# Kernel tuning notes

Hardware: AMD Instinct MI355X
Metric: run time of the kernel (lower is better)

## Reference

```python
import jax, jax.numpy as jnp
import numpy as np

EMB = 768
HEADS = 8
B, N = 8, 1024

def _ln(x, g, b, eps=1e-5):
    mu = jnp.mean(x, axis=-1, keepdims=True)
    var = jnp.mean(jnp.square(x - mu), axis=-1, keepdims=True)
    return (x - mu) * jax.lax.rsqrt(var + eps) * g + b

def setup_inputs() -> dict:
    key = jax.random.key(0)
    ks = jax.random.split(key, 8)
    s_in = 0.02
    return {
        "x": jax.random.normal(ks[0], (B, N, EMB), jnp.float32),
        "w_qkvr": jax.random.normal(ks[1], (EMB, 4 * EMB), jnp.float32) * s_in,
        "b_qkvr": jnp.zeros((4 * EMB,), jnp.float32),
        "w_proj": jax.random.normal(ks[2], (EMB, EMB), jnp.float32) * s_in,
        "b_proj": jnp.zeros((EMB,), jnp.float32),
        "ln1_g": jnp.ones((EMB,), jnp.float32),
        "ln1_b": jnp.zeros((EMB,), jnp.float32),
        "w_ff1": jax.random.normal(ks[3], (EMB, 4 * EMB), jnp.float32) * s_in,
        "b_ff1": jnp.zeros((4 * EMB,), jnp.float32),
        "w_ff2": jax.random.normal(ks[4], (4 * EMB, EMB), jnp.float32) * s_in,
        "b_ff2": jnp.zeros((EMB,), jnp.float32),
        "ln2_g": jnp.ones((EMB,), jnp.float32),
        "ln2_b": jnp.zeros((EMB,), jnp.float32),
    }

def reference(x, w_qkvr, b_qkvr, w_proj, b_proj, ln1_g, ln1_b,
              w_ff1, b_ff1, w_ff2, b_ff2, ln2_g, ln2_b):
    b, n, e = x.shape
    h = HEADS
    d = e // h
    # fused QKV+R projection; einops '(h d qkvr)' => qkvr is the INNERMOST factor
    qkvr = (x @ w_qkvr + b_qkvr).reshape(b, n, h, d, 4)
    qkvr = jnp.transpose(qkvr, (4, 0, 2, 1, 3))  # [4, b, h, n, d]
    q, k, v, r = qkvr[0], qkvr[1], qkvr[2], qkvr[3]
    energy = jnp.einsum('bhqd,bhkd->bhqk', q, k)
    # quirk: softmax of UNSCALED logits, then divide by sqrt(emb_size) AFTER
    att = jax.nn.softmax(energy, axis=-1) / jnp.sqrt(jnp.float32(e))
    out = jnp.einsum('bhqk,bhkd->bhqd', att, v)
    out = out * r  # elementwise r-gate
    out = jnp.transpose(out, (0, 2, 1, 3)).reshape(b, n, e)
    out = out @ w_proj + b_proj
    x1 = _ln(out + x, ln1_g, ln1_b)  # residual then post-LayerNorm
    ff = jax.nn.gelu(x1 @ w_ff1 + b_ff1, approximate=False) @ w_ff2 + b_ff2
    return _ln(ff + x1, ln2_g, ln2_b)
```

## Files before the change

### kernel.cpp

```cpp
#include <hip/hip_runtime.h>
#include <math.h>


typedef __bf16 bf16_t;
typedef __bf16 bf16x4 __attribute__((ext_vector_type(4)));
typedef __bf16 bf16x8 __attribute__((ext_vector_type(8)));
typedef float f32x4 __attribute__((ext_vector_type(4)));

#define EMB   768
#define HEADS 8
#define DHEAD 96
#define BATCH 8
#define SEQ   1024
#define ROWS  (BATCH * SEQ)

__device__ __forceinline__ void load16_lds(const bf16_t* g, bf16_t* l) {
    __builtin_amdgcn_global_load_lds(
        (__attribute__((address_space(1))) unsigned int*)g,
        (__attribute__((address_space(3))) unsigned int*)l,
        16, 0, 0);
}


__global__ void cvt_bf16_kernel(const float* __restrict__ in, bf16_t* __restrict__ out, int n) {
    int stride = gridDim.x * blockDim.x;
    for (int i = blockIdx.x * blockDim.x + threadIdx.x; i < n; i += stride)
        out[i] = (bf16_t)in[i];
}

__global__ void transpose_cvt_kernel(const float* __restrict__ in, bf16_t* __restrict__ out,
                                     int K, int N) {
    __shared__ float t[32][33];
    int n0 = blockIdx.x * 32, k0 = blockIdx.y * 32;
    int tx = threadIdx.x, ty0 = threadIdx.y;
#pragma unroll
    for (int i = 0; i < 4; i++) {
        int ty = ty0 + 8 * i;
        t[ty][tx] = in[(size_t)(k0 + ty) * N + n0 + tx];
    }
    __syncthreads();
#pragma unroll
    for (int i = 0; i < 4; i++) {
        int ty = ty0 + 8 * i;
        out[(size_t)(n0 + ty) * K + k0 + tx] = (bf16_t)t[tx][ty];
    }
}

__global__ void qkvr_transpose_kernel(const float* __restrict__ in, bf16_t* __restrict__ out) {
    __shared__ float t[32][33];
    int n0 = blockIdx.x * 32, k0 = blockIdx.y * 32;
    int tx = threadIdx.x, ty0 = threadIdx.y;
    const int which = n0 / 768, hd0 = n0 % 768;
#pragma unroll
    for (int i = 0; i < 4; i++) {
        int ty = ty0 + 8 * i;
        t[ty][tx] = in[(size_t)(k0 + ty) * 3072 + (hd0 + tx) * 4 + which];
    }
    __syncthreads();
#pragma unroll
    for (int i = 0; i < 4; i++) {
        int ty = ty0 + 8 * i;
        out[(size_t)(n0 + ty) * 768 + k0 + tx] = (bf16_t)t[tx][ty];
    }
}


enum { EPI_QKVR = 0, EPI_PROJ = 1, EPI_GELU = 2, EPI_FF2 = 3 };

#define VMW6 asm volatile("s_waitcnt vmcnt(6)" ::: "memory")
#define VMW0 asm volatile("s_waitcnt vmcnt(0)" ::: "memory")
#define VMNONE do {} while (0)

#define RD8(KC, LB) do { \
    _Pragma("unroll") for (int u = 0; u < 4; u++) { \
        af[u]  = *reinterpret_cast<const bf16x8*>((LB) + aoff[KC][u]); \
        bfr[u] = *reinterpret_cast<const bf16x8*>((LB) + boff[KC][u]); \
    } \
} while (0)

#define MM16() do { \
    __builtin_amdgcn_s_setprio(1); \
    _Pragma("unroll") for (int tr = 0; tr < 4; tr++) \
        _Pragma("unroll") for (int tc = 0; tc < 4; tc++) \
            acc[tr][tc] = __builtin_amdgcn_mfma_f32_16x16x32_bf16( \
                af[tr], bfr[tc], acc[tr][tc], 0, 0, 0); \
    __builtin_amdgcn_s_setprio(0); \
} while (0)

#define STAGE6(DB) do { \
    bf16_t* db_ = lds + (DB) * 24576; \
    _Pragma("unroll") for (int i2 = 0; i2 < 4; i2++) { load16_lds(pa[i2], db_ + lA[i2]); pa[i2] += 64; } \
    _Pragma("unroll") for (int i2 = 0; i2 < 2; i2++) { load16_lds(pb[i2], db_ + lB[i2]); pb[i2] += 64; } \
} while (0)

#define TILE1(BUF, DOSTAGE, GATE, DOBAR) do { \
    const char* lb_ = (const char*)lds + (BUF) * 49152; \
    bf16x8 af[4], bfr[4]; \
    RD8(0, lb_); \
    if (DOSTAGE) STAGE6(((BUF) + 2) % 3); \
    MM16(); \
    RD8(1, lb_); \
    MM16(); \
    GATE; \
    if (DOBAR) { __builtin_amdgcn_sched_barrier(0); __builtin_amdgcn_s_barrier(); } \
} while (0)

template <int EPI, int KSTRIDE, int NKT, int NBX>
__global__ __launch_bounds__(512, 2) void gemmsb_kernel(
    const bf16_t* __restrict__ A,
    const bf16_t* __restrict__ BT,
    const float* __restrict__ bias,
    bf16_t* __restrict__ qo, bf16_t* __restrict__ ko,
    bf16_t* __restrict__ vTo, bf16_t* __restrict__ ro,
    const float* __restrict__ resid,
    float* __restrict__ outf,
    bf16_t* __restrict__ outb)
{
    __shared__ __align__(16) bf16_t lds[3 * 24576];

    const int tid  = threadIdx.x;
    const int wave = tid >> 6, lane = tid & 63;
    const int quad = lane >> 4, col16 = lane & 15;
    const int wrow = (wave >> 1) * 64, wcol = (wave & 1) * 64;

    const int cpx  = gridDim.x >> 3;
    const int id   = blockIdx.x;
    const int wgid = (id & 7) * cpx + (id >> 3);
    const int bx = wgid % NBX, by = wgid / NBX;
    const int m0 = by * 256, n0 = bx * 128;

    int aoff[2][4], boff[2][4];
#pragma unroll
    for (int kc = 0; kc < 2; kc++) {
#pragma unroll
        for (int u = 0; u < 4; u++) {
            const int R = wrow + u * 16 + col16;
            aoff[kc][u] = R * 128 + (((kc * 4 + quad) ^ (R & 7)) * 16);
            const int S = wcol + u * 16 + col16;
            boff[kc][u] = 32768 + S * 128 + (((kc * 4 + quad) ^ (S & 7)) * 16);
        }
    }

    const bf16_t* pa[4]; const bf16_t* pb[2];
    int lA[4], lB[2];
#pragma unroll
    for (int i = 0; i < 4; i++) {
        const int u = tid + 512 * i;
        const int r = u >> 3, j = (u & 7) ^ (r & 7);
        pa[i] = A + (size_t)(m0 + r) * KSTRIDE + j * 8;
        lA[i] = u * 8;
    }
#pragma unroll
    for (int i = 0; i < 2; i++) {
        const int u = tid + 512 * i;
        const int r = u >> 3, j = (u & 7) ^ (r & 7);
        pb[i] = BT + (size_t)(n0 + r) * KSTRIDE + j * 8;
        lB[i] = 16384 + u * 8;
    }

    f32x4 acc[4][4] = {};

    STAGE6(0); STAGE6(1);
    VMW6; __builtin_amdgcn_s_barrier();

#pragma unroll 1
    for (int tg = 0; tg < NKT / 3 - 1; ++tg) {
        TILE1(0, 1, VMW6, 1);
        TILE1(1, 1, VMW6, 1);
        TILE1(2, 1, VMW6, 1);
    }
    TILE1(0, 1, VMW6, 1);
    TILE1(1, 0, VMW0, 1);
    TILE1(2, 0, VMNONE, 0);

    if (EPI == EPI_QKVR) {
        const int whichb = bx / 6;
        if (whichb == 2) {
#pragma unroll
            for (int tr = 0; tr < 4; tr++) {
#pragma unroll
                for (int tc = 0; tc < 4; tc++) {
                    const int hd   = (bx % 6) * 128 + wcol + tc * 16 + col16;
                    const int head = hd / DHEAD, dd = hd % DHEAD;
                    const float bv = bias[hd * 4 + 2];
                    const int row0 = m0 + wrow + tr * 16 + quad * 4;
                    const int b = row0 >> 10, nn0 = row0 & 1023;
                    bf16x4 w;
#pragma unroll
                    for (int rg = 0; rg < 4; rg++) w[rg] = (bf16_t)(acc[tr][tc][rg] + bv);
                    *reinterpret_cast<bf16x4*>(
                        vTo + ((size_t)(b * HEADS + head) * DHEAD + dd) * SEQ + nn0) = w;
                }
            }
        } else {
            bf16_t* dst = (whichb == 0) ? qo : (whichb == 1) ? ko : ro;
#pragma unroll
            for (int tr = 0; tr < 4; tr++) {
#pragma unroll
                for (int tc = 0; tc < 4; tc++) {
                    const int hd   = (bx % 6) * 128 + wcol + tc * 16 + col16;
                    const int head = hd / DHEAD, dd = hd % DHEAD;
                    const float bv = bias[hd * 4 + whichb];
#pragma unroll
                    for (int rg = 0; rg < 4; rg++) {
                        const int row = m0 + wrow + tr * 16 + quad * 4 + rg;
                        const int b = row >> 10, nn = row & 1023;
                        dst[((size_t)(b * HEADS + head) * SEQ + nn) * DHEAD + dd] =
                            (bf16_t)(acc[tr][tc][rg] + bv);
                    }
                }
            }
        }
    } else {
#pragma unroll
        for (int tr = 0; tr < 4; tr++) {
#pragma unroll
            for (int tc = 0; tc < 4; tc++) {
#pragma unroll
                for (int rg = 0; rg < 4; rg++) {
                    const int row  = m0 + wrow + tr * 16 + quad * 4 + rg;
                    const int colg = n0 + wcol + tc * 16 + col16;
                    float v = acc[tr][tc][rg] + bias[colg];
                    if (EPI == EPI_PROJ || EPI == EPI_FF2) {
                        outf[(size_t)row * EMB + colg] = v + resid[(size_t)row * EMB + colg];
                    } else {
                        const float z = 1.5957691216057308f * v * (1.0f + 0.044715f * v * v);
                        const float g = v / (1.0f + __expf(-z));
                        outb[(size_t)row * 3072 + colg] = (bf16_t)g;
                    }
                }
            }
        }
    }
}


__global__ __launch_bounds__(256) void attn_kernel(
    const bf16_t* __restrict__ q, const bf16_t* __restrict__ k,
    const bf16_t* __restrict__ vT, const bf16_t* __restrict__ r,
    bf16_t* __restrict__ attn_out)
{
    __shared__ __align__(16) bf16_t Ks[64 * 96];
    __shared__ __align__(16) bf16_t Vs[96 * 64];
    __shared__ __align__(16) bf16_t P[4][16 * 72];

    const int tid = threadIdx.x, wave = tid >> 6, lane = tid & 63;
    const int quad = lane >> 4, col = lane & 15;
    const int bh = blockIdx.x & 63, qb = blockIdx.x >> 6;
    const int n0 = qb * 64 + wave * 16;
    const bf16_t* qp = q  + (size_t)bh * SEQ * DHEAD;
    const bf16_t* kb = k  + (size_t)bh * SEQ * DHEAD;
    const bf16_t* vb = vT + (size_t)bh * DHEAD * SEQ;
    bf16_t* Pw = P[wave];

    bf16x8 qf[3];
#pragma unroll
    for (int ks = 0; ks < 3; ks++)
        qf[ks] = *reinterpret_cast<const bf16x8*>(qp + (size_t)(n0 + col) * DHEAD + ks * 32 + quad * 8);

    const int u0 = tid, u1 = tid + 256, u2 = tid + 512;
    const int vf0 = u0 >> 3, vp0 = (u0 & 7) ^ (vf0 & 7);
    const int vf1 = u1 >> 3, vp1 = (u1 & 7) ^ (vf1 & 7);
    const int vf2 = u2 >> 3, vp2 = (u2 & 7) ^ (vf2 & 7);

    f32x4 O[6] = {};
    float lsum = 0.f;

    for (int ch = 0; ch < SEQ / 64; ch++) {
        const int kc0 = ch * 64;
        __syncthreads();
        const bf16_t* ksrc = kb + (size_t)kc0 * DHEAD;
        load16_lds(ksrc + u0 * 8, Ks + u0 * 8);
        load16_lds(ksrc + u1 * 8, Ks + u1 * 8);
        load16_lds(ksrc + u2 * 8, Ks + u2 * 8);
        load16_lds(vb + (size_t)vf0 * SEQ + kc0 + vp0 * 8, Vs + u0 * 8);
        load16_lds(vb + (size_t)vf1 * SEQ + kc0 + vp1 * 8, Vs + u1 * 8);
        load16_lds(vb + (size_t)vf2 * SEQ + kc0 + vp2 * 8, Vs + u2 * 8);
        __syncthreads();

        f32x4 s[4] = {};
#pragma unroll
        for (int ks = 0; ks < 3; ks++) {
#pragma unroll
            for (int h = 0; h < 4; h++) {
                bf16x8 kf = *reinterpret_cast<const bf16x8*>(Ks + (h * 16 + col) * DHEAD + ks * 32 + quad * 8);
                s[h] = __builtin_amdgcn_mfma_f32_16x16x32_bf16(kf, qf[ks], s[h], 0, 0, 0);
            }
        }
#pragma unroll
        for (int h = 0; h < 4; h++) {
            bf16x4 w;
#pragma unroll
            for (int rg = 0; rg < 4; rg++) {
                const float e = __expf(s[h][rg]);
                lsum += e;
                w[rg] = (bf16_t)e;
            }
            *reinterpret_cast<bf16x4*>(Pw + col * 72 + h * 16 + quad * 4) = w;
        }
        bf16x8 af0 = *reinterpret_cast<const bf16x8*>(Pw + col * 72 + quad * 8);
        bf16x8 af1 = *reinterpret_cast<const bf16x8*>(Pw + col * 72 + 32 + quad * 8);
#pragma unroll
        for (int tc = 0; tc < 6; tc++) {
            const int feat = tc * 16 + col;
            bf16x8 bv0 = *reinterpret_cast<const bf16x8*>(Vs + feat * 64 + ((quad)     ^ (col & 7)) * 8);
            bf16x8 bv1 = *reinterpret_cast<const bf16x8*>(Vs + feat * 64 + ((4 + quad) ^ (col & 7)) * 8);
            O[tc] = __builtin_amdgcn_mfma_f32_16x16x32_bf16(af0, bv0, O[tc], 0, 0, 0);
            O[tc] = __builtin_amdgcn_mfma_f32_16x16x32_bf16(af1, bv1, O[tc], 0, 0, 0);
        }
    }

    lsum += __shfl_xor(lsum, 16);
    lsum += __shfl_xor(lsum, 32);

    const float inv_sqrt_emb = 0.036084391824351615f;
    const int b = bh >> 3, h = bh & 7;
#pragma unroll
    for (int rg = 0; rg < 4; rg++) {
        const int nrow = quad * 4 + rg;
        const float lr = __shfl(lsum, nrow);
        const float scale = inv_sqrt_emb / lr;
        const int n = n0 + nrow;
#pragma unroll
        for (int tc = 0; tc < 6; tc++) {
            const int feat = tc * 16 + col;
            const float rv = (float)r[((size_t)bh * SEQ + n) * DHEAD + feat];
            attn_out[((size_t)(b * SEQ + n)) * EMB + h * DHEAD + feat] = (bf16_t)(O[tc][rg] * scale * rv);
        }
    }
}


__global__ __launch_bounds__(256) void ln_kernel(
    const float* __restrict__ in, const float* __restrict__ g, const float* __restrict__ b,
    float* __restrict__ y, bf16_t* __restrict__ yb)
{
    const int row = blockIdx.x * 4 + (threadIdx.x >> 6);
    const int lane = threadIdx.x & 63;
    const float* rp = in + (size_t)row * EMB;
    float v[12];
    float sum = 0.f;
#pragma unroll
    for (int i = 0; i < 12; i++) { v[i] = rp[lane + i * 64]; sum += v[i]; }
#pragma unroll
    for (int off = 32; off; off >>= 1) sum += __shfl_xor(sum, off);
    const float mean = sum * (1.0f / 768.0f);
    float s2 = 0.f;
#pragma unroll
    for (int i = 0; i < 12; i++) { float d = v[i] - mean; s2 += d * d; }
#pragma unroll
    for (int off = 32; off; off >>= 1) s2 += __shfl_xor(s2, off);
    const float inv = rsqrtf(s2 * (1.0f / 768.0f) + 1e-5f);
#pragma unroll
    for (int i = 0; i < 12; i++) {
        const int c = lane + i * 64;
        const float o = (v[i] - mean) * inv * g[c] + b[c];
        y[(size_t)row * EMB + c] = o;
        if (yb) yb[(size_t)row * EMB + c] = (bf16_t)o;
    }
}


extern "C" void kernel_launch(void* const* d_in, const int* in_sizes, int n_in,
                              void* d_out, int out_size, void* d_ws, size_t ws_size,
                              hipStream_t stream)
{
    const float* x      = (const float*)d_in[0];
    const float* w_qkvr = (const float*)d_in[1];
    const float* b_qkvr = (const float*)d_in[2];
    const float* w_proj = (const float*)d_in[3];
    const float* b_proj = (const float*)d_in[4];
    const float* ln1_g  = (const float*)d_in[5];
    const float* ln1_b  = (const float*)d_in[6];
    const float* w_ff1  = (const float*)d_in[7];
    const float* b_ff1  = (const float*)d_in[8];
    const float* w_ff2  = (const float*)d_in[9];
    const float* b_ff2  = (const float*)d_in[10];
    const float* ln2_g  = (const float*)d_in[11];
    const float* ln2_b  = (const float*)d_in[12];
    float* out = (float*)d_out;

    char* ws = (char*)d_ws;
    size_t off = 0;
    auto alloc = [&](size_t bytes) {
        char* p = ws + off;
        off += (bytes + 255) & ~(size_t)255;
        return (void*)p;
    };
    const size_t ACT = (size_t)ROWS * EMB;
    bf16_t* xb      = (bf16_t*)alloc(ACT * 2);
    bf16_t* wqkvrT  = (bf16_t*)alloc((size_t)3072 * 768 * 2);
    bf16_t* wprojT  = (bf16_t*)alloc((size_t)768 * 768 * 2);
    bf16_t* wff1T   = (bf16_t*)alloc((size_t)3072 * 768 * 2);
    bf16_t* wff2T   = (bf16_t*)alloc((size_t)768 * 3072 * 2);
    bf16_t* qbuf    = (bf16_t*)alloc(ACT * 2);
    bf16_t* kbuf    = (bf16_t*)alloc(ACT * 2);
    bf16_t* vTbuf   = (bf16_t*)alloc(ACT * 2);
    bf16_t* rbuf    = (bf16_t*)alloc(ACT * 2);
    bf16_t* attn_o  = (bf16_t*)alloc(ACT * 2);
    float*  x1f     = (float*)alloc(ACT * 4);
    bf16_t* x1b     = (bf16_t*)alloc(ACT * 2);
    bf16_t* ff1     = (bf16_t*)alloc((size_t)ROWS * 3072 * 2);
    float*  res     = out;

    dim3 tb32(32, 8);

    cvt_bf16_kernel<<<2048, 256, 0, stream>>>(x, xb, (int)ACT);
    qkvr_transpose_kernel<<<dim3(3072 / 32, 768 / 32), tb32, 0, stream>>>(w_qkvr, wqkvrT);
    transpose_cvt_kernel<<<dim3(768 / 32, 768 / 32), tb32, 0, stream>>>(w_proj, wprojT, 768, 768);
    transpose_cvt_kernel<<<dim3(3072 / 32, 768 / 32), tb32, 0, stream>>>(w_ff1, wff1T, 768, 3072);
    transpose_cvt_kernel<<<dim3(768 / 32, 3072 / 32), tb32, 0, stream>>>(w_ff2, wff2T, 3072, 768);

    gemmsb_kernel<EPI_QKVR, 768, 12, 24><<<768, 512, 0, stream>>>(
        xb, wqkvrT, b_qkvr, qbuf, kbuf, vTbuf, rbuf, nullptr, nullptr, nullptr);

    attn_kernel<<<dim3(SEQ / 64 * BATCH * HEADS), 256, 0, stream>>>(qbuf, kbuf, vTbuf, rbuf, attn_o);

    gemmsb_kernel<EPI_PROJ, 768, 12, 6><<<192, 512, 0, stream>>>(
        attn_o, wprojT, b_proj, nullptr, nullptr, nullptr, nullptr, x, res, nullptr);
    ln_kernel<<<2048, 256, 0, stream>>>(res, ln1_g, ln1_b, x1f, x1b);

    gemmsb_kernel<EPI_GELU, 768, 12, 24><<<768, 512, 0, stream>>>(
        x1b, wff1T, b_ff1, nullptr, nullptr, nullptr, nullptr, nullptr, nullptr, ff1);

    gemmsb_kernel<EPI_FF2, 3072, 48, 6><<<192, 512, 0, stream>>>(
        ff1, wff2T, b_ff2, nullptr, nullptr, nullptr, nullptr, x1f, res, nullptr);
    ln_kernel<<<2048, 256, 0, stream>>>(res, ln2_g, ln2_b, out, nullptr);

    (void)in_sizes; (void)n_in; (void)out_size; (void)ws_size;
}
```

Before: 384.5 us.

## Split-K the FF2 GEMM, fuse partial reduction into LayerNorm, merge prep kernels

The FF2 GEMM (K=3072) previously ran only 192 workgroups. It now uses a 4-way split-K across 768 workgroups. Split 0 writes bias plus residual to the output, and the other splits write raw partials into a reused workspace region (the dead xb..attn_o buffers). The final LayerNorm sums the four partial buffers while it normalizes, and is vectorized with float4. All the conversion and transpose prep kernels are merged into a single launch. The change trades under-occupancy of the long-K GEMM for about 75 MB of extra partial-sum traffic.

```diff
diff --git a/kernel.cpp b/kernel.cpp
--- a/kernel.cpp
+++ b/kernel.cpp
@@ -13,6 +13,7 @@
 #define BATCH 8
 #define SEQ   1024
 #define ROWS  (BATCH * SEQ)
+#define ACTN  ((size_t)ROWS * EMB)
 
 __device__ __forceinline__ void load16_lds(const bf16_t* g, bf16_t* l) {
     __builtin_amdgcn_global_load_lds(
@@ -22,17 +23,10 @@
 }
 
 
-__global__ void cvt_bf16_kernel(const float* __restrict__ in, bf16_t* __restrict__ out, int n) {
-    int stride = gridDim.x * blockDim.x;
-    for (int i = blockIdx.x * blockDim.x + threadIdx.x; i < n; i += stride)
-        out[i] = (bf16_t)in[i];
-}
-
-__global__ void transpose_cvt_kernel(const float* __restrict__ in, bf16_t* __restrict__ out,
-                                     int K, int N) {
-    __shared__ float t[32][33];
-    int n0 = blockIdx.x * 32, k0 = blockIdx.y * 32;
-    int tx = threadIdx.x, ty0 = threadIdx.y;
+__device__ __forceinline__ void tile_transpose(
+    const float* __restrict__ in, bf16_t* __restrict__ out,
+    int K, int N, int n0, int k0, float (*t)[33], int tx, int ty0)
+{
 #pragma unroll
     for (int i = 0; i < 4; i++) {
         int ty = ty0 + 8 * i;
@@ -46,21 +40,58 @@
     }
 }
 
-__global__ void qkvr_transpose_kernel(const float* __restrict__ in, bf16_t* __restrict__ out) {
+__global__ __launch_bounds__(256) void prep_kernel(
+    const float* __restrict__ x, bf16_t* __restrict__ xb,
+    const float* __restrict__ w_qkvr, bf16_t* __restrict__ wqkvrT,
+    const float* __restrict__ w_proj, bf16_t* __restrict__ wprojT,
+    const float* __restrict__ w_ff1, bf16_t* __restrict__ wff1T,
+    const float* __restrict__ w_ff2, bf16_t* __restrict__ wff2T)
+{
     __shared__ float t[32][33];
-    int n0 = blockIdx.x * 32, k0 = blockIdx.y * 32;
-    int tx = threadIdx.x, ty0 = threadIdx.y;
-    const int which = n0 / 768, hd0 = n0 % 768;
-#pragma unroll
-    for (int i = 0; i < 4; i++) {
-        int ty = ty0 + 8 * i;
-        t[ty][tx] = in[(size_t)(k0 + ty) * 3072 + (hd0 + tx) * 4 + which];
-    }
-    __syncthreads();
-#pragma unroll
-    for (int i = 0; i < 4; i++) {
-        int ty = ty0 + 8 * i;
-        out[(size_t)(n0 + ty) * 768 + k0 + tx] = (bf16_t)t[tx][ty];
+    int id = blockIdx.x;
+    if (id < 768) {
+        const int n4 = (int)(ACTN / 4);
+        const int stride = 768 * 256;
+        for (int i = id * 256 + threadIdx.x; i < n4; i += stride) {
+            const float4 v = ((const float4*)x)[i];
+            bf16x4 o;
+            o[0] = (bf16_t)v.x; o[1] = (bf16_t)v.y;
+            o[2] = (bf16_t)v.z; o[3] = (bf16_t)v.w;
+            ((bf16x4*)xb)[i] = o;
+        }
+        return;
+    }
+    id -= 768;
+    const int tx = threadIdx.x & 31, ty0 = threadIdx.x >> 5;
+    if (id < 2304) {
+        const int n0 = (id % 96) * 32, k0 = (id / 96) * 32;
+        const int which = n0 / 768, hd0 = n0 % 768;
+#pragma unroll
+        for (int i = 0; i < 4; i++) {
+            int ty = ty0 + 8 * i;
+            t[ty][tx] = w_qkvr[(size_t)(k0 + ty) * 3072 + (hd0 + tx) * 4 + which];
+        }
+        __syncthreads();
+#pragma unroll
+        for (int i = 0; i < 4; i++) {
+            int ty = ty0 + 8 * i;
+            wqkvrT[(size_t)(n0 + ty) * 768 + k0 + tx] = (bf16_t)t[tx][ty];
+        }
+        return;
+    }
+    id -= 2304;
+    if (id < 576) {
+        tile_transpose(w_proj, wprojT, 768, 768, (id % 24) * 32, (id / 24) * 32, t, tx, ty0);
+        return;
+    }
+    id -= 576;
+    if (id < 2304) {
+        tile_transpose(w_ff1, wff1T, 768, 3072, (id % 96) * 32, (id / 96) * 32, t, tx, ty0);
+        return;
+    }
+    id -= 2304;
+    {
+        tile_transpose(w_ff2, wff2T, 3072, 768, (id % 24) * 32, (id / 24) * 32, t, tx, ty0);
     }
 }
 
@@ -105,7 +136,7 @@
     if (DOBAR) { __builtin_amdgcn_sched_barrier(0); __builtin_amdgcn_s_barrier(); } \
 } while (0)
 
-template <int EPI, int KSTRIDE, int NKT, int NBX>
+template <int EPI, int KSTRIDE, int NKT, int NBX, int SPLITS>
 __global__ __launch_bounds__(512, 2) void gemmsb_kernel(
     const bf16_t* __restrict__ A,
     const bf16_t* __restrict__ BT,
@@ -114,7 +145,8 @@
     bf16_t* __restrict__ vTo, bf16_t* __restrict__ ro,
     const float* __restrict__ resid,
     float* __restrict__ outf,
-    bf16_t* __restrict__ outb)
+    bf16_t* __restrict__ outb,
+    float* __restrict__ pbase)
 {
     __shared__ __align__(16) bf16_t lds[3 * 24576];
 
@@ -125,9 +157,17 @@
 
     const int cpx  = gridDim.x >> 3;
     const int id   = blockIdx.x;
-    const int wgid = (id & 7) * cpx + (id >> 3);
+    int wgid = (id & 7) * cpx + (id >> 3);
+    int split = 0;
+    if (SPLITS > 1) {
+        constexpr int bps = 32 * NBX;
+        split = wgid / bps;
+        wgid -= split * bps;
+    }
     const int bx = wgid % NBX, by = wgid / NBX;
     const int m0 = by * 256, n0 = bx * 128;
+    const bf16_t* Ab = A  + (size_t)split * (NKT * 64);
+    const bf16_t* Bb = BT + (size_t)split * (NKT * 64);
 
     int aoff[2][4], boff[2][4];
 #pragma unroll
@@ -147,14 +187,14 @@
     for (int i = 0; i < 4; i++) {
         const int u = tid + 512 * i;
         const int r = u >> 3, j = (u & 7) ^ (r & 7);
-        pa[i] = A + (size_t)(m0 + r) * KSTRIDE + j * 8;
+        pa[i] = Ab + (size_t)(m0 + r) * KSTRIDE + j * 8;
         lA[i] = u * 8;
     }
 #pragma unroll
     for (int i = 0; i < 2; i++) {
         const int u = tid + 512 * i;
         const int r = u >> 3, j = (u & 7) ^ (r & 7);
-        pb[i] = BT + (size_t)(n0 + r) * KSTRIDE + j * 8;
+        pb[i] = Bb + (size_t)(n0 + r) * KSTRIDE + j * 8;
         lB[i] = 16384 + u * 8;
     }
 
@@ -220,13 +260,17 @@
                 for (int rg = 0; rg < 4; rg++) {
                     const int row  = m0 + wrow + tr * 16 + quad * 4 + rg;
                     const int colg = n0 + wcol + tc * 16 + col16;
-                    float v = acc[tr][tc][rg] + bias[colg];
-                    if (EPI == EPI_PROJ || EPI == EPI_FF2) {
-                        outf[(size_t)row * EMB + colg] = v + resid[(size_t)row * EMB + colg];
-                    } else {
+                    const float a = acc[tr][tc][rg];
+                    if (EPI == EPI_GELU) {
+                        const float v = a + bias[colg];
                         const float z = 1.5957691216057308f * v * (1.0f + 0.044715f * v * v);
                         const float g = v / (1.0f + __expf(-z));
                         outb[(size_t)row * 3072 + colg] = (bf16_t)g;
+                    } else if (SPLITS > 1 && split > 0) {
+                        pbase[(size_t)(split - 1) * ACTN + (size_t)row * EMB + colg] = a;
+                    } else {
+                        outf[(size_t)row * EMB + colg] =
+                            a + bias[colg] + resid[(size_t)row * EMB + colg];
                     }
                 }
             }
@@ -332,31 +376,57 @@
 
 
 __global__ __launch_bounds__(256) void ln_kernel(
-    const float* __restrict__ in, const float* __restrict__ g, const float* __restrict__ b,
+    const float* __restrict__ in, const float* __restrict__ in2,
+    const float* __restrict__ in3, const float* __restrict__ in4,
+    const float* __restrict__ g, const float* __restrict__ b,
     float* __restrict__ y, bf16_t* __restrict__ yb)
 {
     const int row = blockIdx.x * 4 + (threadIdx.x >> 6);
     const int lane = threadIdx.x & 63;
-    const float* rp = in + (size_t)row * EMB;
-    float v[12];
+    const float4* rp  = (const float4*)(in + (size_t)row * EMB);
+    const float4* rp2 = in2 ? (const float4*)(in2 + (size_t)row * EMB) : nullptr;
+    const float4* rp3 = in3 ? (const float4*)(in3 + (size_t)row * EMB) : nullptr;
+    const float4* rp4 = in4 ? (const float4*)(in4 + (size_t)row * EMB) : nullptr;
+    float4 v[3];
     float sum = 0.f;
 #pragma unroll
-    for (int i = 0; i < 12; i++) { v[i] = rp[lane + i * 64]; sum += v[i]; }
+    for (int i = 0; i < 3; i++) {
+        float4 t = rp[lane + i * 64];
+        if (in2) { float4 a = rp2[lane + i * 64]; t.x += a.x; t.y += a.y; t.z += a.z; t.w += a.w; }
+        if (in3) { float4 a = rp3[lane + i * 64]; t.x += a.x; t.y += a.y; t.z += a.z; t.w += a.w; }
+        if (in4) { float4 a = rp4[lane + i * 64]; t.x += a.x; t.y += a.y; t.z += a.z; t.w += a.w; }
+        v[i] = t;
+        sum += t.x + t.y + t.z + t.w;
+    }
 #pragma unroll
     for (int off = 32; off; off >>= 1) sum += __shfl_xor(sum, off);
     const float mean = sum * (1.0f / 768.0f);
     float s2 = 0.f;
 #pragma unroll
-    for (int i = 0; i < 12; i++) { float d = v[i] - mean; s2 += d * d; }
+    for (int i = 0; i < 3; i++) {
+        float dx = v[i].x - mean, dy = v[i].y - mean, dz = v[i].z - mean, dw = v[i].w - mean;
+        s2 += dx * dx + dy * dy + dz * dz + dw * dw;
+    }
 #pragma unroll
     for (int off = 32; off; off >>= 1) s2 += __shfl_xor(s2, off);
     const float inv = rsqrtf(s2 * (1.0f / 768.0f) + 1e-5f);
-#pragma unroll
-    for (int i = 0; i < 12; i++) {
-        const int c = lane + i * 64;
-        const float o = (v[i] - mean) * inv * g[c] + b[c];
-        y[(size_t)row * EMB + c] = o;
-        if (yb) yb[(size_t)row * EMB + c] = (bf16_t)o;
+    const float4* g4 = (const float4*)g;
+    const float4* b4 = (const float4*)b;
+#pragma unroll
+    for (int i = 0; i < 3; i++) {
+        const int c4 = lane + i * 64;
+        const float4 gg = g4[c4], bb = b4[c4];
+        float4 o;
+        o.x = (v[i].x - mean) * inv * gg.x + bb.x;
+        o.y = (v[i].y - mean) * inv * gg.y + bb.y;
+        o.z = (v[i].z - mean) * inv * gg.z + bb.z;
+        o.w = (v[i].w - mean) * inv * gg.w + bb.w;
+        ((float4*)(y + (size_t)row * EMB))[c4] = o;
+        if (yb) {
+            bf16x4 ob;
+            ob[0] = (bf16_t)o.x; ob[1] = (bf16_t)o.y; ob[2] = (bf16_t)o.z; ob[3] = (bf16_t)o.w;
+            *reinterpret_cast<bf16x4*>(yb + (size_t)row * EMB + c4 * 4) = ob;
+        }
     }
 }
 
@@ -387,45 +457,41 @@
         off += (bytes + 255) & ~(size_t)255;
         return (void*)p;
     };
-    const size_t ACT = (size_t)ROWS * EMB;
-    bf16_t* xb      = (bf16_t*)alloc(ACT * 2);
     bf16_t* wqkvrT  = (bf16_t*)alloc((size_t)3072 * 768 * 2);
     bf16_t* wprojT  = (bf16_t*)alloc((size_t)768 * 768 * 2);
     bf16_t* wff1T   = (bf16_t*)alloc((size_t)3072 * 768 * 2);
     bf16_t* wff2T   = (bf16_t*)alloc((size_t)768 * 3072 * 2);
-    bf16_t* qbuf    = (bf16_t*)alloc(ACT * 2);
-    bf16_t* kbuf    = (bf16_t*)alloc(ACT * 2);
-    bf16_t* vTbuf   = (bf16_t*)alloc(ACT * 2);
-    bf16_t* rbuf    = (bf16_t*)alloc(ACT * 2);
-    bf16_t* attn_o  = (bf16_t*)alloc(ACT * 2);
-    float*  x1f     = (float*)alloc(ACT * 4);
-    bf16_t* x1b     = (bf16_t*)alloc(ACT * 2);
+    float*  x1f     = (float*)alloc(ACTN * 4);
+    bf16_t* x1b     = (bf16_t*)alloc(ACTN * 2);
     bf16_t* ff1     = (bf16_t*)alloc((size_t)ROWS * 3072 * 2);
+    bf16_t* xb      = (bf16_t*)alloc(ACTN * 2);
+    bf16_t* qbuf    = (bf16_t*)alloc(ACTN * 2);
+    bf16_t* kbuf    = (bf16_t*)alloc(ACTN * 2);
+    bf16_t* vTbuf   = (bf16_t*)alloc(ACTN * 2);
+    bf16_t* rbuf    = (bf16_t*)alloc(ACTN * 2);
+    bf16_t* attn_o  = (bf16_t*)alloc(ACTN * 2);
     float*  res     = out;
-
-    dim3 tb32(32, 8);
-
-    cvt_bf16_kernel<<<2048, 256, 0, stream>>>(x, xb, (int)ACT);
-    qkvr_transpose_kernel<<<dim3(3072 / 32, 768 / 32), tb32, 0, stream>>>(w_qkvr, wqkvrT);
-    transpose_cvt_kernel<<<dim3(768 / 32, 768 / 32), tb32, 0, stream>>>(w_proj, wprojT, 768, 768);
-    transpose_cvt_kernel<<<dim3(3072 / 32, 768 / 32), tb32, 0, stream>>>(w_ff1, wff1T, 768, 3072);
-    transpose_cvt_kernel<<<dim3(768 / 32, 3072 / 32), tb32, 0, stream>>>(w_ff2, wff2T, 3072, 768);
-
-    gemmsb_kernel<EPI_QKVR, 768, 12, 24><<<768, 512, 0, stream>>>(
-        xb, wqkvrT, b_qkvr, qbuf, kbuf, vTbuf, rbuf, nullptr, nullptr, nullptr);
+    float*  pbase   = (float*)xb;
+
+    prep_kernel<<<8256, 256, 0, stream>>>(x, xb, w_qkvr, wqkvrT, w_proj, wprojT,
+                                          w_ff1, wff1T, w_ff2, wff2T);
+
+    gemmsb_kernel<EPI_QKVR, 768, 12, 24, 1><<<768, 512, 0, stream>>>(
+        xb, wqkvrT, b_qkvr, qbuf, kbuf, vTbuf, rbuf, nullptr, nullptr, nullptr, nullptr);
 
     attn_kernel<<<dim3(SEQ / 64 * BATCH * HEADS), 256, 0, stream>>>(qbuf, kbuf, vTbuf, rbuf, attn_o);
 
-    gemmsb_kernel<EPI_PROJ, 768, 12, 6><<<192, 512, 0, stream>>>(
-        attn_o, wprojT, b_proj, nullptr, nullptr, nullptr, nullptr, x, res, nullptr);
-    ln_kernel<<<2048, 256, 0, stream>>>(res, ln1_g, ln1_b, x1f, x1b);
-
-    gemmsb_kernel<EPI_GELU, 768, 12, 24><<<768, 512, 0, stream>>>(
-        x1b, wff1T, b_ff1, nullptr, nullptr, nullptr, nullptr, nullptr, nullptr, ff1);
-
-    gemmsb_kernel<EPI_FF2, 3072, 48, 6><<<192, 512, 0, stream>>>(
-        ff1, wff2T, b_ff2, nullptr, nullptr, nullptr, nullptr, x1f, res, nullptr);
-    ln_kernel<<<2048, 256, 0, stream>>>(res, ln2_g, ln2_b, out, nullptr);
+    gemmsb_kernel<EPI_PROJ, 768, 12, 6, 1><<<192, 512, 0, stream>>>(
+        attn_o, wprojT, b_proj, nullptr, nullptr, nullptr, nullptr, x, res, nullptr, nullptr);
+    ln_kernel<<<2048, 256, 0, stream>>>(res, nullptr, nullptr, nullptr, ln1_g, ln1_b, x1f, x1b);
+
+    gemmsb_kernel<EPI_GELU, 768, 12, 24, 1><<<768, 512, 0, stream>>>(
+        x1b, wff1T, b_ff1, nullptr, nullptr, nullptr, nullptr, nullptr, nullptr, ff1, nullptr);
+
+    gemmsb_kernel<EPI_FF2, 3072, 12, 6, 4><<<768, 512, 0, stream>>>(
+        ff1, wff2T, b_ff2, nullptr, nullptr, nullptr, nullptr, x1f, res, nullptr, pbase);
+    ln_kernel<<<2048, 256, 0, stream>>>(res, pbase, pbase + ACTN, pbase + 2 * ACTN,
+                                        ln2_g, ln2_b, out, nullptr);
 
     (void)in_sizes; (void)n_in; (void)out_size; (void)ws_size;
 }
```

After: 415.5 us. 8.1% more time.
